# Optimization experiments

Hardware: AMD Instinct MI355X
Metric: run time of the kernel (lower is better)

The kernel has to match this reference:

```python
import jax, jax.numpy as jnp
import numpy as np

# Fixed ViT-B geometry and pool config (match init_kwargs)
P_CLS, L_CLS, K_CLS = 20, 5, 5
P_IMG, L_IMG, K_IMG = 20, 5, 5
P_LEN_CLS = P_CLS * L_CLS          # 100
P_LEN_IMG = P_IMG * L_IMG          # 100
P_LEN = P_LEN_CLS + P_LEN_IMG      # 200
N_TOK = 197                        # 1 cls + 196 patches
N_HEADS = 12
S = N_TOK + P_LEN                  # 397
DIM = 768


def _l2norm(v):
    n = jnp.sqrt(jnp.sum(v * v, axis=-1, keepdims=True))
    return v / jnp.maximum(n, 1e-12)


def _pool(tokens, keys, k):
    # tokens: [N, D], keys: [P, D]
    sim = _l2norm(tokens) @ _l2norm(keys).T            # [N, P]
    vals, idx = jax.lax.top_k(sim, k)                  # gather(sim, topk_idx) == vals
    dist = (1.0 - vals).mean()
    return dist, idx


def setup_inputs() -> dict:
    key = jax.random.key(0)
    k1, k2, k3 = jax.random.split(key, 3)
    x = jax.random.normal(k1, (128, N_TOK, DIM), dtype=jnp.float32)
    keys_cls = jax.random.normal(k2, (12, P_CLS, DIM), dtype=jnp.float32)
    keys_image = jax.random.normal(k3, (12, P_IMG, DIM), dtype=jnp.float32)
    return {"x": x, "keys_cls": keys_cls, "keys_image": keys_image, "layer": 3}


def reference(x, keys_cls, keys_image, layer):
    B = x.shape[0]
    # Base mask rows: cls row sees cls-prompts only; image rows see image-prompts only.
    row_cls = jnp.ones((S,), jnp.float32).at[1 + P_LEN_CLS:1 + P_LEN].set(0.0)
    row_img = jnp.ones((S,), jnp.float32).at[1:1 + P_LEN_CLS].set(0.0)
    base = jnp.concatenate([row_cls[None, :], jnp.tile(row_img, (N_TOK - 1, 1))], axis=0)  # [197, S]
    mask = jnp.broadcast_to(base, (B, N_HEADS, N_TOK, S))

    # CLS token routing -> one-hot over cls pool, expanded per prompt token
    dist_cls, idx_cls = _pool(x[:, 0, :], keys_cls[layer], K_CLS)
    oh_cls = jnp.zeros((B, P_CLS), jnp.float32).at[jnp.arange(B)[:, None], idx_cls].set(1.0)
    tmp_cls = jnp.repeat(oh_cls, L_CLS, axis=1)        # [B, P_LEN_CLS]
    mask = mask.at[:, :, 0, 1:1 + P_LEN_CLS].set(tmp_cls[:, None, :])

    # Image token routing -> per-token one-hot over image pool
    img = x[:, 1:, :].reshape(-1, DIM)                 # [B*196, D]
    dist_img, idx_img = _pool(img, keys_image[layer], K_IMG)
    oh_img = jnp.zeros((B * (N_TOK - 1), P_IMG), jnp.float32)
    oh_img = oh_img.at[jnp.arange(B * (N_TOK - 1))[:, None], idx_img].set(1.0)
    tmp_img = jnp.repeat(oh_img.reshape(B, N_TOK - 1, P_IMG), L_IMG, axis=2)  # [B,196,P_LEN_IMG]
    mask = mask.at[:, :, 1:, 1 + P_LEN_CLS:1 + P_LEN].set(tmp_img[:, None, :, :])

    return mask, dist_cls + dist_img
```

## Files before the change

### kernel.cpp

```cpp
#include <hip/hip_runtime.h>

#define NTOK 197
#define NHEADS 12
#define DIM 768
#define PP 20
#define KK 5
#define LL 5
#define STOT 397
#define BB 128

static const long long MASK_ELEMS = (long long)BB * NHEADS * NTOK * STOT;

__global__ void knorm_kernel(const float* __restrict__ kc,
                             const float* __restrict__ ki,
                             const int* __restrict__ layer_p,
                             float* __restrict__ invn ) {
    int layer = *layer_p;
    int kid = blockIdx.x;
    const float* base = (kid < PP ? kc : ki) + (size_t)layer * PP * DIM;
    const float* kp = base + (size_t)(kid % PP) * DIM;
    int lane = threadIdx.x;
    float s = 0.f;
    for (int i = lane; i < DIM; i += 64) { float v = kp[i]; s += v * v; }
    #pragma unroll
    for (int m = 1; m < 64; m <<= 1) s += __shfl_xor(s, m, 64);
    if (lane == 0) invn[kid] = 1.0f / fmaxf(sqrtf(s), 1e-12f);
}

__global__ __launch_bounds__(256) void route_mask_kernel(
        const float* __restrict__ x,
        const float* __restrict__ kc,
        const float* __restrict__ ki,
        const int* __restrict__ layer_p,
        const float* __restrict__ invn,
        float* __restrict__ out,
        float* __restrict__ dist_ws ) {
    const int t = blockIdx.x;
    const int b = blockIdx.y;
    const int tok = b * NTOK + t;
    const int tid = threadIdx.x;
    const int lane = tid & 63;
    const int wv = tid >> 6;
    const int layer = *layer_p;
    const bool is_cls = (t == 0);

    const float* kb = (is_cls ? kc : ki) + (size_t)layer * PP * DIM;
    const float* invk = invn + (is_cls ? 0 : PP);
    const float* xr = x + (size_t)tok * DIM;

    float xv0 = xr[tid], xv1 = xr[tid + 256], xv2 = xr[tid + 512];
    float xsq = xv0 * xv0 + xv1 * xv1 + xv2 * xv2;
    float acc[PP];
    #pragma unroll
    for (int p = 0; p < PP; ++p) {
        const float* kp = kb + p * DIM;
        acc[p] = xv0 * kp[tid] + xv1 * kp[tid + 256] + xv2 * kp[tid + 512];
    }

    #pragma unroll
    for (int m = 1; m < 64; m <<= 1) {
        xsq += __shfl_xor(xsq, m, 64);
        #pragma unroll
        for (int p = 0; p < PP; ++p) acc[p] += __shfl_xor(acc[p], m, 64);
    }

    __shared__ float red[4][PP + 1];
    __shared__ int bits_sh;
    if (lane == 0) {
        #pragma unroll
        for (int p = 0; p < PP; ++p) red[wv][p] = acc[p];
        red[wv][PP] = xsq;
    }
    __syncthreads();

    if (tid == 0) {
        float xs = red[0][PP] + red[1][PP] + red[2][PP] + red[3][PP];
        float invx = 1.0f / fmaxf(sqrtf(xs), 1e-12f);
        float sims[PP];
        #pragma unroll
        for (int p = 0; p < PP; ++p)
            sims[p] = (red[0][p] + red[1][p] + red[2][p] + red[3][p]) * invx * invk[p];
        int bits = 0;
        float sum5 = 0.f;
        for (int j = 0; j < KK; ++j) {
            int bi = 0; float bv = -3.0e38f;
            for (int p = 0; p < PP; ++p) {
                if (!((bits >> p) & 1) && sims[p] > bv) { bv = sims[p]; bi = p; }
            }
            bits |= (1 << bi);
            sum5 += bv;
        }
        bits_sh = bits;
        dist_ws[tok] = (float)KK - sum5;
    }
    __syncthreads();
    const int bits = bits_sh;

    const size_t hstride = (size_t)NTOK * STOT;
    const size_t rowbase = ((size_t)(b * NHEADS) * NTOK + t) * (size_t)STOT;
    for (int s = tid; s < STOT; s += 256) {
        float v;
        if (is_cls) {
            v = (s == 0) ? 1.0f
              : (s <= 100 ? (float)((bits >> ((s - 1) / 5)) & 1)
              : (s <= 200 ? 0.0f : 1.0f));
        } else {
            v = (s == 0) ? 1.0f
              : (s <= 100 ? 0.0f
              : (s <= 200 ? (float)((bits >> ((s - 101) / 5)) & 1) : 1.0f));
        }
        #pragma unroll
        for (int h = 0; h < NHEADS; ++h) {
            __builtin_nontemporal_store(v, &out[rowbase + (size_t)h * hstride + s]);
        }
    }
}

__global__ void reduce_dist_kernel(const float* __restrict__ dist_ws,
                                   float* __restrict__ out) {
    const int tid = threadIdx.x;
    float sc = 0.f, si = 0.f;
    for (int tok = tid; tok < BB * NTOK; tok += 256) {
        int q = tok / NTOK;
        int r = tok - q * NTOK;
        float v = dist_ws[tok];
        if (r == 0) sc += v; else si += v;
    }
    #pragma unroll
    for (int m = 1; m < 64; m <<= 1) {
        sc += __shfl_xor(sc, m, 64);
        si += __shfl_xor(si, m, 64);
    }
    __shared__ float lc[4], li[4];
    int lane = tid & 63, wv = tid >> 6;
    if (lane == 0) { lc[wv] = sc; li[wv] = si; }
    __syncthreads();
    if (tid == 0) {
        float c = lc[0] + lc[1] + lc[2] + lc[3];
        float i = li[0] + li[1] + li[2] + li[3];
        out[MASK_ELEMS] = c / (float)(BB * KK) + i / (float)(BB * (NTOK - 1) * KK);
    }
}

extern "C" void kernel_launch(void* const* d_in, const int* in_sizes, int n_in,
                              void* d_out, int out_size, void* d_ws, size_t ws_size,
                              hipStream_t stream) {
    const float* x  = (const float*)d_in[0];
    const float* kc = (const float*)d_in[1];
    const float* ki = (const float*)d_in[2];
    const int* layer = (const int*)d_in[3];
    float* out = (float*)d_out;

    float* invn = (float*)d_ws;
    float* dist_ws = (float*)d_ws + 64;

    knorm_kernel<<<40, 64, 0, stream>>>(kc, ki, layer, invn);

    dim3 grid(NTOK, BB);
    route_mask_kernel<<<grid, 256, 0, stream>>>(x, kc, ki, layer, invn, out, dist_ws);

    reduce_dist_kernel<<<1, 256, 0, stream>>>(dist_ws, out);
}
```

Baseline: 185.7 us.

## Split routing and mask writing; thread-per-token routing with vectorized row stores

Routing for image tokens now runs one thread per token, with each thread computing the 20-key dot products serially. This replaces a full 256-thread block per token that needed cross-wave reductions. Mask writing moves to a separate kernel that builds each row once in shared memory and writes it to all 12 heads with 16-byte nontemporal stores. The distance reduction is folded into an extra block of the write kernel. The routing kernel now has only 226 blocks and each thread reads its own x row with strided access, which may leave the GPU underoccupied. Routing results also take a trip through a global workspace.

Result: slower. 359.3 us (+93.5%).

```diff
diff --git a/kernel.cpp b/kernel.cpp
--- a/kernel.cpp
+++ b/kernel.cpp
@@ -5,11 +5,15 @@
 #define DIM 768
 #define PP 20
 #define KK 5
-#define LL 5
 #define STOT 397
 #define BB 128
+#define NIMG 196
+#define NIMGTOK (BB*NIMG)
+#define NALLTOK (BB*NTOK)
 
 static const long long MASK_ELEMS = (long long)BB * NHEADS * NTOK * STOT;
+
+typedef float float4a __attribute__((ext_vector_type(4), aligned(4)));
 
 __global__ void knorm_kernel(const float* __restrict__ kc,
                              const float* __restrict__ ki,
@@ -27,80 +31,158 @@
     if (lane == 0) invn[kid] = 1.0f / fmaxf(sqrtf(s), 1e-12f);
 }
 
-__global__ __launch_bounds__(256) void route_mask_kernel(
+__global__ __launch_bounds__(256) void route_kernel(
         const float* __restrict__ x,
         const float* __restrict__ kc,
         const float* __restrict__ ki,
         const int* __restrict__ layer_p,
         const float* __restrict__ invn,
-        float* __restrict__ out,
-        float* __restrict__ dist_ws ) {
-    const int t = blockIdx.x;
-    const int b = blockIdx.y;
-    const int tok = b * NTOK + t;
+        int* __restrict__ bits_ws,
+        float* __restrict__ dist_ws    ) {
     const int tid = threadIdx.x;
-    const int lane = tid & 63;
-    const int wv = tid >> 6;
     const int layer = *layer_p;
-    const bool is_cls = (t == 0);
-
-    const float* kb = (is_cls ? kc : ki) + (size_t)layer * PP * DIM;
-    const float* invk = invn + (is_cls ? 0 : PP);
-    const float* xr = x + (size_t)tok * DIM;
-
-    float xv0 = xr[tid], xv1 = xr[tid + 256], xv2 = xr[tid + 512];
-    float xsq = xv0 * xv0 + xv1 * xv1 + xv2 * xv2;
-    float acc[PP];
-    #pragma unroll
-    for (int p = 0; p < PP; ++p) {
-        const float* kp = kb + p * DIM;
-        acc[p] = xv0 * kp[tid] + xv1 * kp[tid + 256] + xv2 * kp[tid + 512];
-    }
-
-    #pragma unroll
-    for (int m = 1; m < 64; m <<= 1) {
-        xsq += __shfl_xor(xsq, m, 64);
-        #pragma unroll
-        for (int p = 0; p < PP; ++p) acc[p] += __shfl_xor(acc[p], m, 64);
-    }
-
-    __shared__ float red[4][PP + 1];
-    __shared__ int bits_sh;
-    if (lane == 0) {
-        #pragma unroll
-        for (int p = 0; p < PP; ++p) red[wv][p] = acc[p];
-        red[wv][PP] = xsq;
-    }
-    __syncthreads();
-
-    if (tid == 0) {
-        float xs = red[0][PP] + red[1][PP] + red[2][PP] + red[3][PP];
-        float invx = 1.0f / fmaxf(sqrtf(xs), 1e-12f);
+
+    if (blockIdx.x < 98) {
+        const int i = blockIdx.x * 256 + tid;
+        const int b = i / NIMG;
+        const int tt = i - b * NIMG;
+        const int tok = b * NTOK + 1 + tt;
+        const float* xr = x + (size_t)tok * DIM;
+        const float* kb = ki + (size_t)layer * PP * DIM;
+        const float* ik = invn + PP;
+
+        float acc[PP];
+        #pragma unroll
+        for (int p = 0; p < PP; ++p) acc[p] = 0.f;
+        float xsq = 0.f;
+
+        for (int d0 = 0; d0 < DIM; d0 += 8) {
+            float4 a = *(const float4*)(xr + d0);
+            float4 c = *(const float4*)(xr + d0 + 4);
+            xsq += a.x*a.x + a.y*a.y + a.z*a.z + a.w*a.w
+                 + c.x*c.x + c.y*c.y + c.z*c.z + c.w*c.w;
+            #pragma unroll
+            for (int p = 0; p < PP; ++p) {
+                const float* kp = kb + p * DIM + d0;
+                acc[p] += a.x*kp[0] + a.y*kp[1] + a.z*kp[2] + a.w*kp[3]
+                        + c.x*kp[4] + c.y*kp[5] + c.z*kp[6] + c.w*kp[7];
+            }
+        }
+
+        float invx = 1.0f / fmaxf(sqrtf(xsq), 1e-12f);
         float sims[PP];
         #pragma unroll
-        for (int p = 0; p < PP; ++p)
-            sims[p] = (red[0][p] + red[1][p] + red[2][p] + red[3][p]) * invx * invk[p];
-        int bits = 0;
-        float sum5 = 0.f;
+        for (int p = 0; p < PP; ++p) sims[p] = acc[p] * invx * ik[p];
+
+        int bits = 0; float sum5 = 0.f;
+        #pragma unroll
         for (int j = 0; j < KK; ++j) {
             int bi = 0; float bv = -3.0e38f;
+            #pragma unroll
             for (int p = 0; p < PP; ++p) {
-                if (!((bits >> p) & 1) && sims[p] > bv) { bv = sims[p]; bi = p; }
+                bool ok = !((bits >> p) & 1) && (sims[p] > bv);
+                bv = ok ? sims[p] : bv;
+                bi = ok ? p : bi;
             }
             bits |= (1 << bi);
             sum5 += bv;
         }
-        bits_sh = bits;
+        bits_ws[tok] = bits;
         dist_ws[tok] = (float)KK - sum5;
-    }
-    __syncthreads();
-    const int bits = bits_sh;
-
-    const size_t hstride = (size_t)NTOK * STOT;
-    const size_t rowbase = ((size_t)(b * NHEADS) * NTOK + t) * (size_t)STOT;
+    } else {
+        const int b = blockIdx.x - 98;
+        const int tok = b * NTOK;
+        const int lane = tid & 63;
+        const int wv = tid >> 6;
+        const float* kb = kc + (size_t)layer * PP * DIM;
+        const float* xr = x + (size_t)tok * DIM;
+
+        float xv0 = xr[tid], xv1 = xr[tid + 256], xv2 = xr[tid + 512];
+        float xsq = xv0*xv0 + xv1*xv1 + xv2*xv2;
+        float acc[PP];
+        #pragma unroll
+        for (int p = 0; p < PP; ++p) {
+            const float* kp = kb + p * DIM;
+            acc[p] = xv0*kp[tid] + xv1*kp[tid+256] + xv2*kp[tid+512];
+        }
+        #pragma unroll
+        for (int m = 1; m < 64; m <<= 1) {
+            xsq += __shfl_xor(xsq, m, 64);
+            #pragma unroll
+            for (int p = 0; p < PP; ++p) acc[p] += __shfl_xor(acc[p], m, 64);
+        }
+        __shared__ float red[4][PP + 1];
+        if (lane == 0) {
+            #pragma unroll
+            for (int p = 0; p < PP; ++p) red[wv][p] = acc[p];
+            red[wv][PP] = xsq;
+        }
+        __syncthreads();
+        if (tid == 0) {
+            float xs = red[0][PP] + red[1][PP] + red[2][PP] + red[3][PP];
+            float invx = 1.0f / fmaxf(sqrtf(xs), 1e-12f);
+            float sims[PP];
+            #pragma unroll
+            for (int p = 0; p < PP; ++p)
+                sims[p] = (red[0][p] + red[1][p] + red[2][p] + red[3][p]) * invx * invn[p];
+            int bits = 0; float sum5 = 0.f;
+            for (int j = 0; j < KK; ++j) {
+                int bi = 0; float bv = -3.0e38f;
+                #pragma unroll
+                for (int p = 0; p < PP; ++p) {
+                    bool ok = !((bits >> p) & 1) && (sims[p] > bv);
+                    bv = ok ? sims[p] : bv;
+                    bi = ok ? p : bi;
+                }
+                bits |= (1 << bi);
+                sum5 += bv;
+            }
+            bits_ws[tok] = bits;
+            dist_ws[tok] = (float)KK - sum5;
+        }
+    }
+}
+
+__global__ __launch_bounds__(256) void write_kernel(
+        const int* __restrict__ bits_ws,
+        const float* __restrict__ dist_ws,
+        float* __restrict__ out) {
+    const int bid = blockIdx.x;
+    const int tid = threadIdx.x;
+
+    if (bid == NALLTOK) {
+        float sc = 0.f, si = 0.f;
+        for (int tok = tid; tok < NALLTOK; tok += 256) {
+            int q = tok / NTOK;
+            int r = tok - q * NTOK;
+            float v = dist_ws[tok];
+            if (r == 0) sc += v; else si += v;
+        }
+        #pragma unroll
+        for (int m = 1; m < 64; m <<= 1) {
+            sc += __shfl_xor(sc, m, 64);
+            si += __shfl_xor(si, m, 64);
+        }
+        __shared__ float lc[4], li[4];
+        int lane = tid & 63, wv = tid >> 6;
+        if (lane == 0) { lc[wv] = sc; li[wv] = si; }
+        __syncthreads();
+        if (tid == 0) {
+            float c = lc[0] + lc[1] + lc[2] + lc[3];
+            float i = li[0] + li[1] + li[2] + li[3];
+            out[MASK_ELEMS] = c / (float)(BB * KK) + i / (float)(BB * NIMG * KK);
+        }
+        return;
+    }
+
+    const int b = bid / NTOK;
+    const int t = bid - b * NTOK;
+    const int bits = bits_ws[bid];
+
+    __shared__ __align__(16) float row[STOT + 3];
     for (int s = tid; s < STOT; s += 256) {
         float v;
-        if (is_cls) {
+        if (t == 0) {
             v = (s == 0) ? 1.0f
               : (s <= 100 ? (float)((bits >> ((s - 1) / 5)) & 1)
               : (s <= 200 ? 0.0f : 1.0f));
@@ -109,36 +191,23 @@
               : (s <= 100 ? 0.0f
               : (s <= 200 ? (float)((bits >> ((s - 101) / 5)) & 1) : 1.0f));
         }
-        #pragma unroll
-        for (int h = 0; h < NHEADS; ++h) {
-            __builtin_nontemporal_store(v, &out[rowbase + (size_t)h * hstride + s]);
-        }
-    }
-}
-
-__global__ void reduce_dist_kernel(const float* __restrict__ dist_ws,
-                                   float* __restrict__ out) {
-    const int tid = threadIdx.x;
-    float sc = 0.f, si = 0.f;
-    for (int tok = tid; tok < BB * NTOK; tok += 256) {
-        int q = tok / NTOK;
-        int r = tok - q * NTOK;
-        float v = dist_ws[tok];
-        if (r == 0) sc += v; else si += v;
-    }
+        row[s] = v;
+    }
+    __syncthreads();
+
+    const int hl = tid >> 7;
+    const int j  = tid & 127;
+    const size_t hstride = (size_t)NTOK * STOT;
+    float* base = out + ((size_t)(b * NHEADS) * NTOK + t) * (size_t)STOT;
     #pragma unroll
-    for (int m = 1; m < 64; m <<= 1) {
-        sc += __shfl_xor(sc, m, 64);
-        si += __shfl_xor(si, m, 64);
-    }
-    __shared__ float lc[4], li[4];
-    int lane = tid & 63, wv = tid >> 6;
-    if (lane == 0) { lc[wv] = sc; li[wv] = si; }
-    __syncthreads();
-    if (tid == 0) {
-        float c = lc[0] + lc[1] + lc[2] + lc[3];
-        float i = li[0] + li[1] + li[2] + li[3];
-        out[MASK_ELEMS] = c / (float)(BB * KK) + i / (float)(BB * (NTOK - 1) * KK);
+    for (int pass = 0; pass < 6; ++pass) {
+        float* dst = base + (size_t)(pass * 2 + hl) * hstride;
+        if (j < 99) {
+            float4a v = *(const float4a*)&row[4 * j];
+            __builtin_nontemporal_store(v, (float4a*)(dst + 4 * j));
+        } else if (j == 99) {
+            __builtin_nontemporal_store(row[396], dst + 396);
+        }
     }
 }
 
@@ -151,13 +220,11 @@
     const int* layer = (const int*)d_in[3];
     float* out = (float*)d_out;
 
-    float* invn = (float*)d_ws;
-    float* dist_ws = (float*)d_ws + 64;
+    float* invn   = (float*)d_ws;
+    int*   bitsws = (int*)d_ws + 64;
+    float* distws = (float*)d_ws + 64 + NALLTOK;
 
     knorm_kernel<<<40, 64, 0, stream>>>(kc, ki, layer, invn);
-
-    dim3 grid(NTOK, BB);
-    route_mask_kernel<<<grid, 256, 0, stream>>>(x, kc, ki, layer, invn, out, dist_ws);
-
-    reduce_dist_kernel<<<1, 256, 0, stream>>>(dist_ws, out);
-}
+    route_kernel<<<98 + BB, 256, 0, stream>>>(x, kc, ki, layer, invn, bitsws, distws);
+    write_kernel<<<NALLTOK + 1, 256, 0, stream>>>(bitsws, distws, out);
+}
```

## Process 64 tokens per wavefront with LDS-tiled similarity and vectorized mask stores

Applied to the files above, without the earlier changes.

Replaces the per-token 256-thread block with a single-wavefront block that handles 64 tokens. Key and token chunks are staged in LDS so each lane computes one token's similarities without cross-lane reductions. The mask rows are written with 4-wide nontemporal stores, and per-block distance partials shrink the final reduction. The grid drops to a few hundred small blocks, which risks too little occupancy to saturate write bandwidth.

Measured after the change: 239.8 us. 29.2% more time.

```diff
diff --git a/kernel.cpp b/kernel.cpp
--- a/kernel.cpp
+++ b/kernel.cpp
@@ -5,11 +5,20 @@
 #define DIM 768
 #define PP 20
 #define KK 5
-#define LL 5
 #define STOT 397
 #define BB 128
+#define NIMG 196
+#define NIMGBLK 392
+#define NBLK 394
+#define CHUNK 128
+#define NCHUNK 6
+#define PITCH 132
+#define HSTRIDE (NTOK * STOT)
 
 static const long long MASK_ELEMS = (long long)BB * NHEADS * NTOK * STOT;
+
+typedef float float4a __attribute__((ext_vector_type(4), aligned(4)));
+typedef float float4b __attribute__((ext_vector_type(4), aligned(16)));
 
 __global__ void knorm_kernel(const float* __restrict__ kc,
                              const float* __restrict__ ki,
@@ -27,119 +36,150 @@
     if (lane == 0) invn[kid] = 1.0f / fmaxf(sqrtf(s), 1e-12f);
 }
 
-__global__ __launch_bounds__(256) void route_mask_kernel(
+__global__ __launch_bounds__(64) void fused_kernel(
         const float* __restrict__ x,
         const float* __restrict__ kc,
         const float* __restrict__ ki,
         const int* __restrict__ layer_p,
         const float* __restrict__ invn,
         float* __restrict__ out,
-        float* __restrict__ dist_ws ) {
-    const int t = blockIdx.x;
-    const int b = blockIdx.y;
-    const int tok = b * NTOK + t;
-    const int tid = threadIdx.x;
-    const int lane = tid & 63;
-    const int wv = tid >> 6;
+        float* __restrict__ dist_part ) {
+    const int blk = blockIdx.x;
+    const int lane = threadIdx.x;
+    const bool is_cls = (blk >= NIMGBLK);
     const int layer = *layer_p;
-    const bool is_cls = (t == 0);
-
+
+    __shared__ float xs[64 * PITCH];
+    __shared__ float ks[PP * PITCH];
+    __shared__ int rowoff[64];
+    __shared__ int obase[64];
+    __shared__ int bitsarr[64];
+
+    if (!is_cls) {
+        int i = blk * 64 + lane;
+        int b = i / NIMG;
+        int t = i - b * NIMG;
+        rowoff[lane] = (b * NTOK + 1 + t) * DIM;
+        obase[lane]  = (b * (NHEADS * NTOK) + 1 + t) * STOT;
+    } else {
+        int b = (blk - NIMGBLK) * 64 + lane;
+        rowoff[lane] = (b * NTOK) * DIM;
+        obase[lane]  = (b * (NHEADS * NTOK)) * STOT;
+    }
     const float* kb = (is_cls ? kc : ki) + (size_t)layer * PP * DIM;
-    const float* invk = invn + (is_cls ? 0 : PP);
-    const float* xr = x + (size_t)tok * DIM;
-
-    float xv0 = xr[tid], xv1 = xr[tid + 256], xv2 = xr[tid + 512];
-    float xsq = xv0 * xv0 + xv1 * xv1 + xv2 * xv2;
+    const float* ik = invn + (is_cls ? 0 : PP);
+    __syncthreads();
+
     float acc[PP];
     #pragma unroll
-    for (int p = 0; p < PP; ++p) {
-        const float* kp = kb + p * DIM;
-        acc[p] = xv0 * kp[tid] + xv1 * kp[tid + 256] + xv2 * kp[tid + 512];
-    }
-
-    #pragma unroll
-    for (int m = 1; m < 64; m <<= 1) {
-        xsq += __shfl_xor(xsq, m, 64);
+    for (int p = 0; p < PP; ++p) acc[p] = 0.f;
+    float xsq = 0.f;
+
+    for (int c = 0; c < NCHUNK; ++c) {
         #pragma unroll
-        for (int p = 0; p < PP; ++p) acc[p] += __shfl_xor(acc[p], m, 64);
-    }
-
-    __shared__ float red[4][PP + 1];
-    __shared__ int bits_sh;
-    if (lane == 0) {
+        for (int pass = 0; pass < 10; ++pass) {
+            int idx = pass * 64 + lane;
+            int kr = idx >> 5, f4 = idx & 31;
+            float4b v = *(const float4b*)(kb + kr * DIM + c * CHUNK + f4 * 4);
+            *(float4b*)&ks[kr * PITCH + f4 * 4] = v;
+        }
+        #pragma unroll 8
+        for (int pass = 0; pass < 32; ++pass) {
+            int idx = pass * 64 + lane;
+            int r = idx >> 5, f4 = idx & 31;
+            float4b v = *(const float4b*)(x + rowoff[r] + c * CHUNK + f4 * 4);
+            *(float4b*)&xs[r * PITCH + f4 * 4] = v;
+        }
+        __syncthreads();
+        #pragma unroll 2
+        for (int q = 0; q < 32; ++q) {
+            float4b xv = *(const float4b*)&xs[lane * PITCH + q * 4];
+            xsq += xv.x * xv.x + xv.y * xv.y + xv.z * xv.z + xv.w * xv.w;
+            #pragma unroll
+            for (int p = 0; p < PP; ++p) {
+                float4b kv = *(const float4b*)&ks[p * PITCH + q * 4];
+                acc[p] += xv.x * kv.x + xv.y * kv.y + xv.z * kv.z + xv.w * kv.w;
+            }
+        }
+        __syncthreads();
+    }
+
+    float invx = 1.0f / fmaxf(sqrtf(xsq), 1e-12f);
+    float sims[PP];
+    #pragma unroll
+    for (int p = 0; p < PP; ++p) sims[p] = acc[p] * invx * ik[p];
+    int bits = 0; float sum5 = 0.f;
+    #pragma unroll
+    for (int j = 0; j < KK; ++j) {
+        int bi = 0; float bv = -3.0e38f;
         #pragma unroll
-        for (int p = 0; p < PP; ++p) red[wv][p] = acc[p];
-        red[wv][PP] = xsq;
-    }
+        for (int p = 0; p < PP; ++p) {
+            bool ok = !((bits >> p) & 1) && (sims[p] > bv);
+            bv = ok ? sims[p] : bv;
+            bi = ok ? p : bi;
+        }
+        bits |= (1 << bi);
+        sum5 += bv;
+    }
+    bitsarr[lane] = bits;
+    float dist = (float)KK - sum5;
+    #pragma unroll
+    for (int m = 1; m < 64; m <<= 1) dist += __shfl_xor(dist, m, 64);
+    if (lane == 0) dist_part[blk] = dist;
     __syncthreads();
 
-    if (tid == 0) {
-        float xs = red[0][PP] + red[1][PP] + red[2][PP] + red[3][PP];
-        float invx = 1.0f / fmaxf(sqrtf(xs), 1e-12f);
-        float sims[PP];
-        #pragma unroll
-        for (int p = 0; p < PP; ++p)
-            sims[p] = (red[0][p] + red[1][p] + red[2][p] + red[3][p]) * invx * invk[p];
-        int bits = 0;
-        float sum5 = 0.f;
-        for (int j = 0; j < KK; ++j) {
-            int bi = 0; float bv = -3.0e38f;
-            for (int p = 0; p < PP; ++p) {
-                if (!((bits >> p) & 1) && sims[p] > bv) { bv = sims[p]; bi = p; }
-            }
-            bits |= (1 << bi);
-            sum5 += bv;
-        }
-        bits_sh = bits;
-        dist_ws[tok] = (float)KK - sum5;
-    }
-    __syncthreads();
-    const int bits = bits_sh;
-
-    const size_t hstride = (size_t)NTOK * STOT;
-    const size_t rowbase = ((size_t)(b * NHEADS) * NTOK + t) * (size_t)STOT;
-    for (int s = tid; s < STOT; s += 256) {
-        float v;
-        if (is_cls) {
-            v = (s == 0) ? 1.0f
-              : (s <= 100 ? (float)((bits >> ((s - 1) / 5)) & 1)
-              : (s <= 200 ? 0.0f : 1.0f));
-        } else {
-            v = (s == 0) ? 1.0f
-              : (s <= 100 ? 0.0f
-              : (s <= 200 ? (float)((bits >> ((s - 101) / 5)) & 1) : 1.0f));
-        }
+    const int s0a = 4 * lane;
+    const int s0b = 256 + 4 * lane;
+    int pidx_a[4], pidx_b[4];
+    float fix_a[4], fix_b[4];
+    const int lo = is_cls ? 1 : 101;
+    #pragma unroll
+    for (int j = 0; j < 4; ++j) {
+        int s = s0a + j;
+        if (s == 0 || s > 200) { pidx_a[j] = -1; fix_a[j] = 1.f; }
+        else if (s >= lo && s < lo + 100) { pidx_a[j] = (s - lo) / 5; fix_a[j] = 0.f; }
+        else { pidx_a[j] = -1; fix_a[j] = 0.f; }
+        s = s0b + j;
+        if (s == 0 || s > 200) { pidx_b[j] = -1; fix_b[j] = 1.f; }
+        else if (s >= lo && s < lo + 100) { pidx_b[j] = (s - lo) / 5; fix_b[j] = 0.f; }
+        else { pidx_b[j] = -1; fix_b[j] = 0.f; }
+    }
+
+    for (int tau = 0; tau < 64; ++tau) {
+        const int tb = bitsarr[tau];
+        float* dst0 = out + (size_t)obase[tau];
+        float4a v0, v1;
+        v0.x = pidx_a[0] < 0 ? fix_a[0] : (float)((tb >> pidx_a[0]) & 1);
+        v0.y = pidx_a[1] < 0 ? fix_a[1] : (float)((tb >> pidx_a[1]) & 1);
+        v0.z = pidx_a[2] < 0 ? fix_a[2] : (float)((tb >> pidx_a[2]) & 1);
+        v0.w = pidx_a[3] < 0 ? fix_a[3] : (float)((tb >> pidx_a[3]) & 1);
+        v1.x = pidx_b[0] < 0 ? fix_b[0] : (float)((tb >> pidx_b[0]) & 1);
+        v1.y = pidx_b[1] < 0 ? fix_b[1] : (float)((tb >> pidx_b[1]) & 1);
+        v1.z = pidx_b[2] < 0 ? fix_b[2] : (float)((tb >> pidx_b[2]) & 1);
+        v1.w = pidx_b[3] < 0 ? fix_b[3] : (float)((tb >> pidx_b[3]) & 1);
         #pragma unroll
         for (int h = 0; h < NHEADS; ++h) {
-            __builtin_nontemporal_store(v, &out[rowbase + (size_t)h * hstride + s]);
-        }
-    }
-}
-
-__global__ void reduce_dist_kernel(const float* __restrict__ dist_ws,
-                                   float* __restrict__ out) {
-    const int tid = threadIdx.x;
-    float sc = 0.f, si = 0.f;
-    for (int tok = tid; tok < BB * NTOK; tok += 256) {
-        int q = tok / NTOK;
-        int r = tok - q * NTOK;
-        float v = dist_ws[tok];
-        if (r == 0) sc += v; else si += v;
-    }
+            float* dst = dst0 + h * HSTRIDE;
+            __builtin_nontemporal_store(v0, (float4a*)(dst + s0a));
+            if (lane < 35) __builtin_nontemporal_store(v1, (float4a*)(dst + s0b));
+            else if (lane == 35) __builtin_nontemporal_store(1.0f, dst + 396);
+        }
+    }
+}
+
+__global__ void reduce_kernel(const float* __restrict__ dist_part,
+                              float* __restrict__ out) {
+    int lane = threadIdx.x;
+    float si = 0.f, sc = 0.f;
+    for (int i = lane; i < NIMGBLK; i += 64) si += dist_part[i];
+    if (lane < 2) sc = dist_part[NIMGBLK + lane];
     #pragma unroll
     for (int m = 1; m < 64; m <<= 1) {
+        si += __shfl_xor(si, m, 64);
         sc += __shfl_xor(sc, m, 64);
-        si += __shfl_xor(si, m, 64);
-    }
-    __shared__ float lc[4], li[4];
-    int lane = tid & 63, wv = tid >> 6;
-    if (lane == 0) { lc[wv] = sc; li[wv] = si; }
-    __syncthreads();
-    if (tid == 0) {
-        float c = lc[0] + lc[1] + lc[2] + lc[3];
-        float i = li[0] + li[1] + li[2] + li[3];
-        out[MASK_ELEMS] = c / (float)(BB * KK) + i / (float)(BB * (NTOK - 1) * KK);
-    }
+    }
+    if (lane == 0)
+        out[MASK_ELEMS] = sc * (1.0f / (BB * KK)) + si * (1.0f / (BB * NIMG * KK));
 }
 
 extern "C" void kernel_launch(void* const* d_in, const int* in_sizes, int n_in,
@@ -152,12 +192,9 @@
     float* out = (float*)d_out;
 
     float* invn = (float*)d_ws;
-    float* dist_ws = (float*)d_ws + 64;
+    float* dpart = (float*)d_ws + 64;
 
     knorm_kernel<<<40, 64, 0, stream>>>(kc, ki, layer, invn);
-
-    dim3 grid(NTOK, BB);
-    route_mask_kernel<<<grid, 256, 0, stream>>>(x, kc, ki, layer, invn, out, dist_ws);
-
-    reduce_dist_kernel<<<1, 256, 0, stream>>>(dist_ws, out);
-}
+    fused_kernel<<<NBLK, 64, 0, stream>>>(x, kc, ki, layer, invn, out, dpart);
+    reduce_kernel<<<1, 64, 0, stream>>>(dpart, out);
+}
```

## Use one-wave blocks with float4 loads, LDS transpose reduction, and vector mask stores

Applied to the files above, without the earlier changes.

Each token is now handled by a single 64-lane block instead of four waves. x and key rows are read as float4, and the 20 dot products are reduced through an LDS transpose instead of per-value shuffles. Top-k runs wave-uniformly over readlane-broadcast sortable integer keys. Mask rows are written with 4-wide stores (only 4-byte aligned) in place of scalar nontemporal stores. This aims to cut instruction count and store transactions on the write-bound mask output, but it drops the nontemporal hint and uses misaligned vector writes.

New measurement: 229.8 us. +23.7%, slower.

```diff
diff --git a/kernel.cpp b/kernel.cpp
--- a/kernel.cpp
+++ b/kernel.cpp
@@ -5,11 +5,20 @@
 #define DIM 768
 #define PP 20
 #define KK 5
-#define LL 5
 #define STOT 397
 #define BB 128
+#define NIMG 196
+#define NALLTOK (BB * NTOK)
+#define HSTRIDE (NTOK * STOT)
 
 static const long long MASK_ELEMS = (long long)BB * NHEADS * NTOK * STOT;
+
+typedef float float4a __attribute__((ext_vector_type(4), aligned(4)));
+typedef float float4b __attribute__((ext_vector_type(4), aligned(16)));
+
+static __device__ __forceinline__ float dot4(float4b a, float4b b) {
+    return a.x * b.x + a.y * b.y + a.z * b.z + a.w * b.w;
+}
 
 __global__ void knorm_kernel(const float* __restrict__ kc,
                              const float* __restrict__ ki,
@@ -27,7 +36,7 @@
     if (lane == 0) invn[kid] = 1.0f / fmaxf(sqrtf(s), 1e-12f);
 }
 
-__global__ __launch_bounds__(256) void route_mask_kernel(
+__global__ __launch_bounds__(64) void fused_kernel(
         const float* __restrict__ x,
         const float* __restrict__ kc,
         const float* __restrict__ ki,
@@ -35,95 +44,118 @@
         const float* __restrict__ invn,
         float* __restrict__ out,
         float* __restrict__ dist_ws ) {
-    const int t = blockIdx.x;
-    const int b = blockIdx.y;
-    const int tok = b * NTOK + t;
-    const int tid = threadIdx.x;
-    const int lane = tid & 63;
-    const int wv = tid >> 6;
+    const int bid = blockIdx.x;
+    const int l = threadIdx.x;
+    const int b = bid / NTOK;
+    const int t = bid - b * NTOK;
+    const bool is_cls = (t == 0);
     const int layer = *layer_p;
-    const bool is_cls = (t == 0);
 
-    const float* kb = (is_cls ? kc : ki) + (size_t)layer * PP * DIM;
-    const float* invk = invn + (is_cls ? 0 : PP);
-    const float* xr = x + (size_t)tok * DIM;
+    const float* __restrict__ kb = (is_cls ? kc : ki) + (size_t)layer * PP * DIM;
+    const float* __restrict__ xr = x + (size_t)bid * DIM;
 
-    float xv0 = xr[tid], xv1 = xr[tid + 256], xv2 = xr[tid + 512];
-    float xsq = xv0 * xv0 + xv1 * xv1 + xv2 * xv2;
+    __shared__ float red[21 * 65 + 64];
+
+    float4b xv0 = *(const float4b*)(xr + 4 * l);
+    float4b xv1 = *(const float4b*)(xr + 256 + 4 * l);
+    float4b xv2 = *(const float4b*)(xr + 512 + 4 * l);
+    float xsq = dot4(xv0, xv0) + dot4(xv1, xv1) + dot4(xv2, xv2);
+
     float acc[PP];
     #pragma unroll
     for (int p = 0; p < PP; ++p) {
         const float* kp = kb + p * DIM;
-        acc[p] = xv0 * kp[tid] + xv1 * kp[tid + 256] + xv2 * kp[tid + 512];
+        float4b k0 = *(const float4b*)(kp + 4 * l);
+        float4b k1 = *(const float4b*)(kp + 256 + 4 * l);
+        float4b k2 = *(const float4b*)(kp + 512 + 4 * l);
+        acc[p] = dot4(xv0, k0) + dot4(xv1, k1) + dot4(xv2, k2);
     }
 
     #pragma unroll
-    for (int m = 1; m < 64; m <<= 1) {
-        xsq += __shfl_xor(xsq, m, 64);
+    for (int v = 0; v < PP; ++v) red[v * 65 + l] = acc[v];
+    red[PP * 65 + l] = xsq;
+    __syncthreads();
+
+    float part = 0.f;
+    if (l < 63) {
+        int r = l / 3;
+        int seg = l - 3 * r;
+        int s0 = seg * 21 + (seg > 0 ? 1 : 0);
+        int n  = 22 - (seg > 0 ? 1 : 0);
+        const float* rr = &red[r * 65 + s0];
         #pragma unroll
-        for (int p = 0; p < PP; ++p) acc[p] += __shfl_xor(acc[p], m, 64);
-    }
-
-    __shared__ float red[4][PP + 1];
-    __shared__ int bits_sh;
-    if (lane == 0) {
-        #pragma unroll
-        for (int p = 0; p < PP; ++p) red[wv][p] = acc[p];
-        red[wv][PP] = xsq;
+        for (int i = 0; i < 22; ++i)
+            if (i < n) part += rr[i];
     }
     __syncthreads();
+    float* red2 = &red[21 * 65];
+    if (l < 63) red2[l] = part;
+    __syncthreads();
 
-    if (tid == 0) {
-        float xs = red[0][PP] + red[1][PP] + red[2][PP] + red[3][PP];
-        float invx = 1.0f / fmaxf(sqrtf(xs), 1e-12f);
-        float sims[PP];
+    float dotv = 0.f;
+    if (l < 21) dotv = red2[3 * l] + red2[3 * l + 1] + red2[3 * l + 2];
+
+    const float* __restrict__ ik = invn + (is_cls ? 0 : PP);
+    float sv = dotv * ((l < PP) ? ik[l] : 1.0f);
+
+    int ibits = __float_as_int(sv);
+    unsigned mu = (ibits < 0) ? ~(unsigned)ibits : ((unsigned)ibits | 0x80000000u);
+
+    unsigned su[PP];
+    #pragma unroll
+    for (int p = 0; p < PP; ++p) su[p] = (unsigned)__builtin_amdgcn_readlane((int)mu, p);
+    float xsqv = __uint_as_float((unsigned)__builtin_amdgcn_readlane(__float_as_int(dotv), PP));
+
+    unsigned bits = 0u;
+    float sum5 = 0.f;
+    #pragma unroll
+    for (int j = 0; j < KK; ++j) {
+        unsigned best = 0u; int bidx = 0;
         #pragma unroll
-        for (int p = 0; p < PP; ++p)
-            sims[p] = (red[0][p] + red[1][p] + red[2][p] + red[3][p]) * invx * invk[p];
-        int bits = 0;
-        float sum5 = 0.f;
-        for (int j = 0; j < KK; ++j) {
-            int bi = 0; float bv = -3.0e38f;
-            for (int p = 0; p < PP; ++p) {
-                if (!((bits >> p) & 1) && sims[p] > bv) { bv = sims[p]; bi = p; }
-            }
-            bits |= (1 << bi);
-            sum5 += bv;
+        for (int p = 0; p < PP; ++p) {
+            bool ok = !((bits >> p) & 1u) && (su[p] > best);
+            best = ok ? su[p] : best;
+            bidx = ok ? p : bidx;
         }
-        bits_sh = bits;
-        dist_ws[tok] = (float)KK - sum5;
+        bits |= (1u << bidx);
+        unsigned fb = (best & 0x80000000u) ? (best & 0x7FFFFFFFu) : ~best;
+        sum5 += __uint_as_float(fb);
     }
-    __syncthreads();
-    const int bits = bits_sh;
+    float invx = 1.0f / fmaxf(sqrtf(xsqv), 1e-12f);
+    if (l == 0) dist_ws[bid] = (float)KK - sum5 * invx;
 
-    const size_t hstride = (size_t)NTOK * STOT;
-    const size_t rowbase = ((size_t)(b * NHEADS) * NTOK + t) * (size_t)STOT;
-    for (int s = tid; s < STOT; s += 256) {
-        float v;
-        if (is_cls) {
-            v = (s == 0) ? 1.0f
-              : (s <= 100 ? (float)((bits >> ((s - 1) / 5)) & 1)
-              : (s <= 200 ? 0.0f : 1.0f));
-        } else {
-            v = (s == 0) ? 1.0f
-              : (s <= 100 ? 0.0f
-              : (s <= 200 ? (float)((bits >> ((s - 101) / 5)) & 1) : 1.0f));
-        }
-        #pragma unroll
-        for (int h = 0; h < NHEADS; ++h) {
-            __builtin_nontemporal_store(v, &out[rowbase + (size_t)h * hstride + s]);
-        }
+    const int lo = is_cls ? 1 : 101;
+    float4a v0;
+    #pragma unroll
+    for (int k = 0; k < 4; ++k) {
+        int s = 4 * l + k;
+        unsigned d = (unsigned)(s - lo);
+        bool inw = d < 100u;
+        unsigned q = d / 5u;
+        float vv = ((s == 0) | (s >= 201)) ? 1.f
+                 : (inw ? (float)((bits >> q) & 1u) : 0.f);
+        v0[k] = vv;
+    }
+    float4a ones = {1.f, 1.f, 1.f, 1.f};
+
+    #pragma unroll
+    for (int h = 0; h < NHEADS; ++h) {
+        float* d0 = out + ((size_t)(b * NHEADS + h) * NTOK + t) * (size_t)STOT;
+        *(float4a*)(d0 + 4 * l) = v0;
+        if (l < 35)      *(float4a*)(d0 + 256 + 4 * l) = ones;
+        else if (l == 35) d0[396] = 1.0f;
     }
 }
 
-__global__ void reduce_dist_kernel(const float* __restrict__ dist_ws,
-                                   float* __restrict__ out) {
+__global__ __launch_bounds__(256) void reduce_kernel(
+        const float* __restrict__ dist_ws,
+        float* __restrict__ out) {
     const int tid = threadIdx.x;
     float sc = 0.f, si = 0.f;
-    for (int tok = tid; tok < BB * NTOK; tok += 256) {
-        int q = tok / NTOK;
-        int r = tok - q * NTOK;
-        float v = dist_ws[tok];
+    for (int i = tid; i < NALLTOK; i += 256) {
+        unsigned q = (unsigned)i / 197u;
+        unsigned r = (unsigned)i - q * 197u;
+        float v = dist_ws[i];
         if (r == 0) sc += v; else si += v;
     }
     #pragma unroll
@@ -138,7 +170,7 @@
     if (tid == 0) {
         float c = lc[0] + lc[1] + lc[2] + lc[3];
         float i = li[0] + li[1] + li[2] + li[3];
-        out[MASK_ELEMS] = c / (float)(BB * KK) + i / (float)(BB * (NTOK - 1) * KK);
+        out[MASK_ELEMS] = c / (float)(BB * KK) + i / (float)(BB * NIMG * KK);
     }
 }
 
@@ -151,13 +183,10 @@
     const int* layer = (const int*)d_in[3];
     float* out = (float*)d_out;
 
-    float* invn = (float*)d_ws;
+    float* invn    = (float*)d_ws;
     float* dist_ws = (float*)d_ws + 64;
 
     knorm_kernel<<<40, 64, 0, stream>>>(kc, ki, layer, invn);
-
-    dim3 grid(NTOK, BB);
-    route_mask_kernel<<<grid, 256, 0, stream>>>(x, kc, ki, layer, invn, out, dist_ws);
-
-    reduce_dist_kernel<<<1, 256, 0, stream>>>(dist_ws, out);
+    fused_kernel<<<NALLTOK, 64, 0, stream>>>(x, kc, ki, layer, invn, out, dist_ws);
+    reduce_kernel<<<1, 256, 0, stream>>>(dist_ws, out);
 }
```
